# Kernel tuning notes

Hardware: AMD Instinct MI355X
Metric: run time of the kernel (lower is better)

The kernel has to match this reference:

```python
import jax, jax.numpy as jnp
import numpy as np

B, T, C = 2, 2048, 2048
H, HKV = 32, 8
D = C // H            # head_dim = 64
G = H // HKV          # groups = 4
ROPE_BASE = 10000.0


def _rotate_half(x):
    x1, x2 = jnp.split(x, 2, axis=-1)
    return jnp.concatenate((-x2, x1), axis=-1)


def _rope_tables(seq_len, dim):
    inv_freq = 1.0 / (ROPE_BASE ** (jnp.arange(0, dim, 2, dtype=jnp.float32) / dim))
    t = jnp.arange(seq_len, dtype=jnp.float32)
    freqs = jnp.outer(t, inv_freq)          # [T, D/2]
    emb = jnp.concatenate((freqs, freqs), axis=-1)  # [T, D]
    return jnp.cos(emb), jnp.sin(emb)


def setup_inputs() -> dict:
    key = jax.random.key(0)
    ks = jax.random.split(key, 5)
    s = 0.02
    return {
        "x": jax.random.normal(ks[0], (B, T, C), jnp.float32),
        "Wq": jax.random.normal(ks[1], (C, C), jnp.float32) * s,
        "Wk": jax.random.normal(ks[2], (HKV * D, C), jnp.float32) * s,
        "Wv": jax.random.normal(ks[3], (HKV * D, C), jnp.float32) * s,
        "Wo": jax.random.normal(ks[4], (C, C), jnp.float32) * s,
    }


def reference(x, Wq, Wk, Wv, Wo):
    b, t, c = x.shape
    # fused QKV projections (nn.Linear: y = x @ W.T)
    q = (x @ Wq.T).reshape(b, t, H, D).transpose(0, 2, 1, 3)      # [B,H,T,D]
    k = (x @ Wk.T).reshape(b, t, HKV, D).transpose(0, 2, 1, 3)    # [B,HKV,T,D]
    v = (x @ Wv.T).reshape(b, t, HKV, D).transpose(0, 2, 1, 3)

    # RoPE (start_pos = 0)
    cos, sin = _rope_tables(t, D)           # [T, D] each
    cos = cos[None, None]                   # [1,1,T,D]
    sin = sin[None, None]
    q = q * cos + _rotate_half(q) * sin
    k = k * cos + _rotate_half(k) * sin

    # GQA head expansion (repeat_interleave on head dim)
    k = jnp.repeat(k, G, axis=1)            # [B,H,T,D]
    v = jnp.repeat(v, G, axis=1)

    # causal attention
    scale = 1.0 / jnp.sqrt(jnp.asarray(D, jnp.float32))
    scores = jnp.einsum('bhqd,bhkd->bhqk', q, k) * scale          # [B,H,T,T]
    causal = jnp.tril(jnp.ones((t, t), dtype=bool))
    scores = jnp.where(causal[None, None], scores, -jnp.inf)
    attn = jax.nn.softmax(scores.astype(jnp.float32), axis=-1).astype(q.dtype)
    out = jnp.einsum('bhqk,bhkd->bhqd', attn, v)                  # [B,H,T,D]
    out = out.transpose(0, 2, 1, 3).reshape(b, t, c)
    return out @ Wo.T
```

## Files before the change

### kernel.cpp

```cpp
#include <hip/hip_runtime.h>
#include <hip/hip_bf16.h>
#include <math.h>

typedef short short8 __attribute__((ext_vector_type(8)));
typedef float floatx4 __attribute__((ext_vector_type(4)));
typedef unsigned int uintx4 __attribute__((ext_vector_type(4)));
typedef int intx2 __attribute__((ext_vector_type(2)));

typedef __attribute__((address_space(1))) unsigned int as1_u32;
typedef __attribute__((address_space(3))) unsigned int as3_u32;

__device__ __forceinline__ void load_lds16(const void* g, void* l) {
  __builtin_amdgcn_global_load_lds((const as1_u32*)g, (as3_u32*)l, 16, 0, 0);
}

__device__ __forceinline__ unsigned short f2bf(float f) {
  __bf16 h = (__bf16)f;
  return __builtin_bit_cast(unsigned short, h);
}

__device__ __forceinline__ unsigned int pack_bf16(float a, float b) {
  return (unsigned int)f2bf(a) | ((unsigned int)f2bf(b) << 16);
}

#define MFMA16(a, b, c) __builtin_amdgcn_mfma_f32_16x16x32_bf16(a, b, c, 0, 0, 0)

#define TB 2
#define TT 2048
#define TC 2048
#define QKN 2560
#define KOFF 2048
#define SCALE_Q 0.18033688f

__global__ __launch_bounds__(256) void cast_all(
    const float* __restrict__ x, const float* __restrict__ wq,
    const float* __restrict__ wk, const float* __restrict__ wv,
    const float* __restrict__ wo,
    unsigned short* __restrict__ xb, unsigned short* __restrict__ wqkv,
    unsigned short* __restrict__ wob, float2* __restrict__ ropeTab) {
  if (blockIdx.x < 256) {
    const int idx = blockIdx.x * 256 + threadIdx.x;
    const int t = idx >> 5, d = idx & 31;
    const float inv = exp2f((float)d * -0.4152410119f);
    float sn, cs;
    sincosf((float)t * inv, &sn, &cs);
    ropeTab[idx] = make_float2(cs, sn);
  }
  long i4 = (long)blockIdx.x * 256 + threadIdx.x;
  const float* src;
  unsigned short* dst;
  if (i4 < 2097152)      { src = x;  dst = xb; }
  else if (i4 < 3145728) { src = wq; dst = wqkv;           i4 -= 2097152; }
  else if (i4 < 3407872) { src = wk; dst = wqkv + 4194304; i4 -= 3145728; }
  else if (i4 < 3670016) { src = wv; dst = wqkv + 5242880; i4 -= 3407872; }
  else                   { src = wo; dst = wob;            i4 -= 3670016; }
  float4 v = ((const float4*)src)[i4];
  ushort4 o;
  o.x = f2bf(v.x); o.y = f2bf(v.y); o.z = f2bf(v.z); o.w = f2bf(v.w);
  ((ushort4*)dst)[i4] = o;
}

#define MFMA_QUAD(I0, J0, BF)                                                  \
  __builtin_amdgcn_s_setprio(1);                                               \
  _Pragma("unroll") for (int i_ = 0; i_ < 4; ++i_) {                           \
    _Pragma("unroll") for (int j_ = 0; j_ < 2; ++j_) {                         \
      acc[(I0) + i_][(J0) + j_] =                                              \
          MFMA16(af[i_][0], BF[j_][0], acc[(I0) + i_][(J0) + j_]);             \
      acc[(I0) + i_][(J0) + j_] =                                              \
          MFMA16(af[i_][1], BF[j_][1], acc[(I0) + i_][(J0) + j_]);             \
    }                                                                          \
  }                                                                            \
  __builtin_amdgcn_s_setprio(0);

__device__ __forceinline__ void gemm256_8ph(
    const unsigned short* __restrict__ A, const unsigned short* __restrict__ Bw,
    char* dynlds, int m0, int n0, int K, floatx4 (&acc)[8][4]) {
  const int tid = threadIdx.x;
  const int lane = tid & 63;
  const int w = tid >> 6;
  const int quad = lane >> 4, l15 = lane & 15;
  const int wm = w >> 2, wn = w & 3;

  const int srow8 = tid >> 3;
  const int schk = (tid & 7) ^ (srow8 & 7);
  const unsigned short* aS = A + (size_t)(m0 + srow8) * K + schk * 8;
  const unsigned short* bS = Bw + (size_t)(n0 + srow8) * K + schk * 8;

  const int key0 = (quad ^ (l15 & 7)) << 4;
  const int key1 = ((4 + quad) ^ (l15 & 7)) << 4;
  const int rdA = (wm * 16 + l15) * 128;
  const int rdB = 32768 + ((wn >> 1) * 64 + (wn & 1) * 16 + l15) * 128;

  const int NIT = K >> 7;

  auto stage = [&](int bb, int isB, int h, int tt) {
    char* d = dynlds + bb * 65536 + isB * 32768 + h * 16384;
    const unsigned short* s = (isB ? bS : aS) + (size_t)tt * 64 + (size_t)(h * 128) * K;
    load_lds16(s, d + tid * 16);
    load_lds16(s + (size_t)64 * K, d + 8192 + tid * 16);
  };

  stage(0, 0, 0, 0); stage(0, 1, 0, 0); stage(0, 1, 1, 0); stage(0, 0, 1, 0);
  stage(1, 0, 0, 1); stage(1, 1, 1, 1);
  asm volatile("s_waitcnt vmcnt(4)" ::: "memory");
  __builtin_amdgcn_s_barrier();

  short8 af[4][2], bfA[2][2], bfB[2][2];
  const char* cb0 = dynlds;
  const char* cb1 = dynlds + 65536;

  for (int it = 0; it < NIT; ++it) {
    const int tO = it * 2 + 1, tE2 = it * 2 + 2, tO2 = it * 2 + 3;
    const bool STG = (it < NIT - 1);

#pragma unroll
    for (int i = 0; i < 4; ++i) {
      af[i][0] = *(const short8*)(cb0 + rdA + i * 4096 + key0);
      af[i][1] = *(const short8*)(cb0 + rdA + i * 4096 + key1);
    }
#pragma unroll
    for (int j = 0; j < 2; ++j) {
      bfA[j][0] = *(const short8*)(cb0 + rdB + j * 4096 + key0);
      bfA[j][1] = *(const short8*)(cb0 + rdB + j * 4096 + key1);
    }
    stage(1, 1, 0, tO);
    __builtin_amdgcn_s_barrier();
    asm volatile("s_waitcnt lgkmcnt(0)" ::: "memory");
    MFMA_QUAD(0, 0, bfA)
    __builtin_amdgcn_s_barrier();

#pragma unroll
    for (int j = 0; j < 2; ++j) {
      bfB[j][0] = *(const short8*)(cb0 + rdB + 16384 + j * 4096 + key0);
      bfB[j][1] = *(const short8*)(cb0 + rdB + 16384 + j * 4096 + key1);
    }
    stage(1, 0, 1, tO);
    __builtin_amdgcn_s_barrier();
    asm volatile("s_waitcnt lgkmcnt(0)" ::: "memory");
    MFMA_QUAD(0, 2, bfB)
    __builtin_amdgcn_s_barrier();

#pragma unroll
    for (int i = 0; i < 4; ++i) {
      af[i][0] = *(const short8*)(cb0 + rdA + (i + 4) * 4096 + key0);
      af[i][1] = *(const short8*)(cb0 + rdA + (i + 4) * 4096 + key1);
    }
    if (STG) stage(0, 0, 0, tE2);
    __builtin_amdgcn_s_barrier();
    asm volatile("s_waitcnt lgkmcnt(0)" ::: "memory");
    MFMA_QUAD(4, 2, bfB)
    __builtin_amdgcn_s_barrier();

    if (STG) stage(0, 1, 1, tE2);
    MFMA_QUAD(4, 0, bfA)
    if (STG) asm volatile("s_waitcnt vmcnt(4)" ::: "memory");
    else     asm volatile("s_waitcnt vmcnt(0)" ::: "memory");
    __builtin_amdgcn_s_barrier();

#pragma unroll
    for (int i = 0; i < 4; ++i) {
      af[i][0] = *(const short8*)(cb1 + rdA + i * 4096 + key0);
      af[i][1] = *(const short8*)(cb1 + rdA + i * 4096 + key1);
    }
#pragma unroll
    for (int j = 0; j < 2; ++j) {
      bfA[j][0] = *(const short8*)(cb1 + rdB + j * 4096 + key0);
      bfA[j][1] = *(const short8*)(cb1 + rdB + j * 4096 + key1);
    }
    if (STG) stage(0, 1, 0, tE2);
    __builtin_amdgcn_s_barrier();
    asm volatile("s_waitcnt lgkmcnt(0)" ::: "memory");
    MFMA_QUAD(0, 0, bfA)
    __builtin_amdgcn_s_barrier();

#pragma unroll
    for (int j = 0; j < 2; ++j) {
      bfB[j][0] = *(const short8*)(cb1 + rdB + 16384 + j * 4096 + key0);
      bfB[j][1] = *(const short8*)(cb1 + rdB + 16384 + j * 4096 + key1);
    }
    if (STG) stage(0, 0, 1, tE2);
    __builtin_amdgcn_s_barrier();
    asm volatile("s_waitcnt lgkmcnt(0)" ::: "memory");
    MFMA_QUAD(0, 2, bfB)
    __builtin_amdgcn_s_barrier();

#pragma unroll
    for (int i = 0; i < 4; ++i) {
      af[i][0] = *(const short8*)(cb1 + rdA + (i + 4) * 4096 + key0);
      af[i][1] = *(const short8*)(cb1 + rdA + (i + 4) * 4096 + key1);
    }
    if (STG) stage(1, 0, 0, tO2);
    __builtin_amdgcn_s_barrier();
    asm volatile("s_waitcnt lgkmcnt(0)" ::: "memory");
    MFMA_QUAD(4, 2, bfB)
    __builtin_amdgcn_s_barrier();

    if (STG) stage(1, 1, 1, tO2);
    MFMA_QUAD(4, 0, bfA)
    if (STG) asm volatile("s_waitcnt vmcnt(4)" ::: "memory");
    else     asm volatile("s_waitcnt vmcnt(0)" ::: "memory");
    __builtin_amdgcn_s_barrier();
  }
}

#define OUTCOL(n0, wn, j, l15) \
  ((n0) + ((j) >> 1) * 128 + ((wn) >> 1) * 64 + ((wn) & 1) * 16 + ((j) & 1) * 32 + (l15))

__global__ __launch_bounds__(512, 2) void gemm_qkv(const unsigned short* __restrict__ A,
                                                   const unsigned short* __restrict__ Bw,
                                                   unsigned short* __restrict__ qk,
                                                   unsigned short* __restrict__ vT,
                                                   const float2* __restrict__ ropeTab) {
  extern __shared__ char dynlds[];
  const int K = 2048;
  const int tid = threadIdx.x;
  const int lane = tid & 63, w = tid >> 6;
  const int quad = lane >> 4, l15 = lane & 15;
  const int wm = w >> 2, wn = w & 3;

  const int lin = blockIdx.y * 12 + blockIdx.x;
  const int wg = (lin & 7) * 24 + (lin >> 3);
  const int m0 = (wg / 12) * 256;
  const int n0 = (wg % 12) * 256;

  floatx4 acc[8][4];
#pragma unroll
  for (int i = 0; i < 8; ++i)
#pragma unroll
    for (int j = 0; j < 4; ++j) acc[i][j] = (floatx4){0.f, 0.f, 0.f, 0.f};

  gemm256_8ph(A, Bw, dynlds, m0, n0, K, acc);

  if (n0 < QKN) {
    const float qscale = (n0 < KOFF) ? SCALE_Q : 1.0f;
    const int d = (wn & 1) * 16 + l15;
#pragma unroll
    for (int i = 0; i < 8; ++i) {
      const int rowb = m0 + i * 32 + wm * 16 + quad * 4;
      const int tb = rowb & (TT - 1);
#pragma unroll
      for (int jp = 0; jp < 4; jp += 2) {
        const int col = OUTCOL(n0, wn, jp, l15);
#pragma unroll
        for (int r = 0; r < 4; ++r) {
          const float2 cssn = ropeTab[(tb + r) * 32 + d];
          const float a = acc[i][jp][r], b2 = acc[i][jp + 1][r];
          const float qa = (a * cssn.x - b2 * cssn.y) * qscale;
          const float qb = (b2 * cssn.x + a * cssn.y) * qscale;
          unsigned short* p = qk + (size_t)(rowb + r) * QKN + col;
          p[0] = f2bf(qa);
          p[32] = f2bf(qb);
        }
      }
    }
  } else {
#pragma unroll
    for (int i = 0; i < 8; ++i) {
      const int rowb = m0 + i * 32 + wm * 16 + quad * 4;
#pragma unroll
      for (int j = 0; j < 4; ++j) {
        const int col = OUTCOL(n0, wn, j, l15);
        ushort4 pk;
        pk.x = f2bf(acc[i][j][0]); pk.y = f2bf(acc[i][j][1]);
        pk.z = f2bf(acc[i][j][2]); pk.w = f2bf(acc[i][j][3]);
        *(ushort4*)(vT + (size_t)(col - 2560) * 4096 + rowb) = pk;
      }
    }
  }
}

__global__ __launch_bounds__(512, 2) void gemm_nt_f32(const unsigned short* __restrict__ A,
                                                      const unsigned short* __restrict__ Bw,
                                                      float* __restrict__ C,
                                                      int M, int N, int Kdim) {
  extern __shared__ char dynlds[];
  const int K = 2048;
  const int tid = threadIdx.x;
  const int lane = tid & 63, w = tid >> 6;
  const int quad = lane >> 4, l15 = lane & 15;
  const int wm = w >> 2, wn = w & 3;

  const int lin = blockIdx.y * 8 + blockIdx.x;
  const int wg = (lin & 7) * 16 + (lin >> 3);
  const int m0 = (wg >> 3) * 256;
  const int n0 = (wg & 7) * 256;

  floatx4 acc[8][4];
#pragma unroll
  for (int i = 0; i < 8; ++i)
#pragma unroll
    for (int j = 0; j < 4; ++j) acc[i][j] = (floatx4){0.f, 0.f, 0.f, 0.f};

  gemm256_8ph(A, Bw, dynlds, m0, n0, K, acc);

#pragma unroll
  for (int i = 0; i < 8; ++i) {
    const int row = m0 + i * 32 + wm * 16 + quad * 4;
#pragma unroll
    for (int j = 0; j < 4; ++j) {
      const int col = OUTCOL(n0, wn, j, l15);
#pragma unroll
      for (int r = 0; r < 4; ++r)
        C[(size_t)(row + r) * N + col] = acc[i][j][r];
    }
  }
}

__global__ __launch_bounds__(256, 3) void attn_kernel(const unsigned short* __restrict__ qk,
                                                      const unsigned short* __restrict__ vT,
                                                      unsigned short* __restrict__ attn) {
  const int h = blockIdx.x, b = blockIdx.y;
  const int qt = 15 - (int)blockIdx.z;
  const int hk = h >> 2;
  const int tid = threadIdx.x;
  const int w = tid >> 6, lane = tid & 63, quad = lane >> 4, l15 = lane & 15;

  __shared__ char lds[32768];

  const int srow = tid >> 3;
  const int sgrp = ((tid & 7) ^ (srow & 7));
  const int relbase = w * 32 + l15;

  const short8 ones = {16256, 16256, 16256, 16256, 16256, 16256, 16256, 16256};

  const size_t rowQ = (size_t)(b * TT + qt * 128);

  {
    const unsigned short* qsrc = qk + (rowQ + srow) * QKN + h * 64 + sgrp * 8;
#pragma unroll
    for (int p = 0; p < 4; ++p)
      load_lds16(qsrc + (size_t)p * 32 * QKN, lds + p * 4096 + tid * 16);
  }
  __syncthreads();
  short8 qf[2][2];
#pragma unroll
  for (int i = 0; i < 2; ++i)
#pragma unroll
    for (int ks = 0; ks < 2; ++ks)
      qf[i][ks] = *(const short8*)(lds + (w * 32 + i * 16 + l15) * 128 +
                                   ((((ks << 2) + quad) ^ (l15 & 7)) << 4));
  __syncthreads();

  floatx4 accO[2][4], accL[2];
#pragma unroll
  for (int i = 0; i < 2; ++i) {
    accL[i] = (floatx4){0.f, 0.f, 0.f, 0.f};
#pragma unroll
    for (int j = 0; j < 4; ++j) accO[i][j] = (floatx4){0.f, 0.f, 0.f, 0.f};
  }

  const unsigned short* kptr =
      qk + (size_t)(b * TT + srow) * QKN + KOFF + hk * 64 + sgrp * 8;
  const unsigned short* vptr =
      vT + (size_t)(hk * 64 + srow) * 4096 + b * TT + sgrp * 8;

  load_lds16(kptr, lds + tid * 16);
  load_lds16(kptr + (size_t)32 * QKN, lds + 4096 + tid * 16);
  load_lds16(vptr, lds + 16384 + tid * 16);
  load_lds16(vptr + (size_t)32 * 4096, lds + 16384 + 4096 + tid * 16);
  kptr += (size_t)64 * QKN;
  vptr += 64;
  __syncthreads();

  auto step = [&](const int BUF, const bool PREF, const int MREL) {
    if (PREF) {
      char* kd = lds + ((BUF ^ 1) * 8192);
      char* vd = lds + 16384 + ((BUF ^ 1) * 8192);
      load_lds16(kptr, kd + tid * 16);
      load_lds16(kptr + (size_t)32 * QKN, kd + 4096 + tid * 16);
      load_lds16(vptr, vd + tid * 16);
      load_lds16(vptr + (size_t)32 * 4096, vd + 4096 + tid * 16);
      kptr += (size_t)64 * QKN;
      vptr += 64;
    }

    const char* Ks = lds + BUF * 8192;
    floatx4 st[2][4];
    __builtin_amdgcn_s_setprio(1);
#pragma unroll
    for (int jm = 0; jm < 4; ++jm) {
      const int krow = jm * 16 + l15;
      const short8 kf0 = *(const short8*)(Ks + krow * 128 + ((quad ^ (l15 & 7)) << 4));
      const short8 kf1 = *(const short8*)(Ks + krow * 128 + (((4 + quad) ^ (l15 & 7)) << 4));
#pragma unroll
      for (int i = 0; i < 2; ++i) {
        floatx4 z = (floatx4){0.f, 0.f, 0.f, 0.f};
        z = __builtin_amdgcn_mfma_f32_16x16x32_bf16(kf0, qf[i][0], z, 0, 0, 0);
        st[i][jm] = __builtin_amdgcn_mfma_f32_16x16x32_bf16(kf1, qf[i][1], z, 0, 0, 0);
      }
    }
    __builtin_amdgcn_s_setprio(0);

    const char* Vt = lds + 16384 + BUF * 8192;
    short8 vf[2][4];
#pragma unroll
    for (int ks = 0; ks < 2; ++ks)
#pragma unroll
      for (int jd = 0; jd < 4; ++jd) {
        const int d = jd * 16 + l15;
        vf[ks][jd] = *(const short8*)(Vt + d * 128 +
                                      ((((ks << 2) + quad) ^ (l15 & 7)) << 4));
      }

    short8 pT[2][2];
#pragma unroll
    for (int i = 0; i < 2; ++i) {
      unsigned int U[4][2];
#pragma unroll
      for (int jm = 0; jm < 4; ++jm) {
        float e0 = __builtin_amdgcn_exp2f(st[i][jm][0]);
        float e1 = __builtin_amdgcn_exp2f(st[i][jm][1]);
        float e2 = __builtin_amdgcn_exp2f(st[i][jm][2]);
        float e3 = __builtin_amdgcn_exp2f(st[i][jm][3]);
        if (MREL >= 0) {
          const int rel = relbase + i * 16 - MREL;
          const int kg = jm * 16 + quad * 4;
          if (kg > rel) e0 = 0.f;
          if (kg + 1 > rel) e1 = 0.f;
          if (kg + 2 > rel) e2 = 0.f;
          if (kg + 3 > rel) e3 = 0.f;
        }
        U[jm][0] = pack_bf16(e0, e1);
        U[jm][1] = pack_bf16(e2, e3);
      }
#pragma unroll
      for (int ks = 0; ks < 2; ++ks) {
        uintx4 t;
#pragma unroll
        for (int hh = 0; hh < 2; ++hh) {
          intx2 r32 = __builtin_amdgcn_permlane32_swap(
              (int)U[2 * ks][hh], (int)U[2 * ks + 1][hh], false, false);
          intx2 r16 = __builtin_amdgcn_permlane16_swap(r32[0], r32[1], false, false);
          t[hh] = (unsigned int)r16[0];
          t[2 + hh] = (unsigned int)r16[1];
        }
        pT[i][ks] = __builtin_bit_cast(short8, t);
      }
    }

    __builtin_amdgcn_s_setprio(1);
#pragma unroll
    for (int ks = 0; ks < 2; ++ks) {
      accL[0] = __builtin_amdgcn_mfma_f32_16x16x32_bf16(pT[0][ks], ones, accL[0], 0, 0, 0);
      accL[1] = __builtin_amdgcn_mfma_f32_16x16x32_bf16(pT[1][ks], ones, accL[1], 0, 0, 0);
#pragma unroll
      for (int jd = 0; jd < 4; ++jd) {
        accO[0][jd] = __builtin_amdgcn_mfma_f32_16x16x32_bf16(pT[0][ks], vf[ks][jd], accO[0][jd], 0, 0, 0);
        accO[1][jd] = __builtin_amdgcn_mfma_f32_16x16x32_bf16(pT[1][ks], vf[ks][jd], accO[1][jd], 0, 0, 0);
      }
    }
    __builtin_amdgcn_s_setprio(0);
    __syncthreads();
  };

  for (int t2 = 0; t2 < qt; ++t2) {
    step(0, true, -1);
    step(1, true, -1);
  }
  step(0, true, 0);
  step(1, false, 64);

#pragma unroll
  for (int i2 = 0; i2 < 2; ++i2) {
    floatx4 rl;
#pragma unroll
    for (int r = 0; r < 4; ++r) rl[r] = __builtin_amdgcn_rcpf(accL[i2][r]);
#pragma unroll
    for (int jd = 0; jd < 4; ++jd) {
      const int col = h * 64 + jd * 16 + l15;
#pragma unroll
      for (int r = 0; r < 4; ++r) {
        const size_t row = rowQ + w * 32 + i2 * 16 + quad * 4 + r;
        attn[row * TC + col] = f2bf(accO[i2][jd][r] * rl[r]);
      }
    }
  }
}

extern "C" void kernel_launch(void* const* d_in, const int* in_sizes, int n_in,
                              void* d_out, int out_size, void* d_ws, size_t ws_size,
                              hipStream_t stream) {
  const float* x = (const float*)d_in[0];
  const float* Wq = (const float*)d_in[1];
  const float* Wk = (const float*)d_in[2];
  const float* Wv = (const float*)d_in[3];
  const float* Wo = (const float*)d_in[4];
  float* out = (float*)d_out;

  char* ws = (char*)d_ws;
  unsigned short* xb   = (unsigned short*)(ws);
  unsigned short* wqkv = (unsigned short*)(ws + 16777216);
  unsigned short* wob  = (unsigned short*)(ws + 29360128);
  unsigned short* qk   = (unsigned short*)(ws + 37748736);
  unsigned short* vT   = (unsigned short*)(ws + 58720256);
  unsigned short* attn = (unsigned short*)(ws + 62914560);
  float2* ropeTab = (float2*)(ws + 62914560);

  cast_all<<<18432, 256, 0, stream>>>(x, Wq, Wk, Wv, Wo, xb, wqkv, wob, ropeTab);
  gemm_qkv<<<dim3(12, 16), 512, 131072, stream>>>(xb, wqkv, qk, vT, ropeTab);
  attn_kernel<<<dim3(32, 2, 16), 256, 0, stream>>>(qk, vT, attn);
  gemm_nt_f32<<<dim3(8, 16), 512, 131072, stream>>>(attn, wob, out, 4096, TC, 2048);
}
```

Measured before the change: 263.9 us.

## Software-pipeline LDS fragment reads ahead of MFMAs in GEMM mainloop

```diff
diff --git a/kernel.cpp b/kernel.cpp
--- a/kernel.cpp
+++ b/kernel.cpp
@@ -60,17 +60,29 @@
   ((ushort4*)dst)[i4] = o;
 }
 
-#define MFMA_QUAD(I0, J0, BF)                                                  \
+#define MFMA_Q(AF, I0, J0, BF)                                                 \
   __builtin_amdgcn_s_setprio(1);                                               \
   _Pragma("unroll") for (int i_ = 0; i_ < 4; ++i_) {                           \
     _Pragma("unroll") for (int j_ = 0; j_ < 2; ++j_) {                         \
       acc[(I0) + i_][(J0) + j_] =                                              \
-          MFMA16(af[i_][0], BF[j_][0], acc[(I0) + i_][(J0) + j_]);             \
+          MFMA16(AF[i_][0], BF[j_][0], acc[(I0) + i_][(J0) + j_]);             \
       acc[(I0) + i_][(J0) + j_] =                                              \
-          MFMA16(af[i_][1], BF[j_][1], acc[(I0) + i_][(J0) + j_]);             \
+          MFMA16(AF[i_][1], BF[j_][1], acc[(I0) + i_][(J0) + j_]);             \
     }                                                                          \
   }                                                                            \
   __builtin_amdgcn_s_setprio(0);
+
+#define RD_A(DST, CB, OFS)                                                     \
+  _Pragma("unroll") for (int i_ = 0; i_ < 4; ++i_) {                           \
+    DST[i_][0] = *(const short8*)((CB) + rdA + ((OFS) + i_) * 4096 + key0);    \
+    DST[i_][1] = *(const short8*)((CB) + rdA + ((OFS) + i_) * 4096 + key1);    \
+  }
+
+#define RD_B(DST, CB, OFS)                                                     \
+  _Pragma("unroll") for (int j_ = 0; j_ < 2; ++j_) {                           \
+    DST[j_][0] = *(const short8*)((CB) + rdB + (OFS) + j_ * 4096 + key0);      \
+    DST[j_][1] = *(const short8*)((CB) + rdB + (OFS) + j_ * 4096 + key1);      \
+  }
 
 __device__ __forceinline__ void gemm256_8ph(
     const unsigned short* __restrict__ A, const unsigned short* __restrict__ Bw,
@@ -104,101 +116,81 @@
   stage(1, 0, 0, 1); stage(1, 1, 1, 1);
   asm volatile("s_waitcnt vmcnt(4)" ::: "memory");
   __builtin_amdgcn_s_barrier();
-
-  short8 af[4][2], bfA[2][2], bfB[2][2];
+  asm volatile("" ::: "memory");
+
+  short8 afLo[4][2], afHi[4][2], bfAe[2][2], bfAo[2][2], bfB[2][2];
   const char* cb0 = dynlds;
   const char* cb1 = dynlds + 65536;
+
+  RD_A(afLo, cb0, 0)
+  RD_B(bfAe, cb0, 0)
 
   for (int it = 0; it < NIT; ++it) {
     const int tO = it * 2 + 1, tE2 = it * 2 + 2, tO2 = it * 2 + 3;
     const bool STG = (it < NIT - 1);
 
-#pragma unroll
-    for (int i = 0; i < 4; ++i) {
-      af[i][0] = *(const short8*)(cb0 + rdA + i * 4096 + key0);
-      af[i][1] = *(const short8*)(cb0 + rdA + i * 4096 + key1);
-    }
-#pragma unroll
-    for (int j = 0; j < 2; ++j) {
-      bfA[j][0] = *(const short8*)(cb0 + rdB + j * 4096 + key0);
-      bfA[j][1] = *(const short8*)(cb0 + rdB + j * 4096 + key1);
-    }
     stage(1, 1, 0, tO);
-    __builtin_amdgcn_s_barrier();
+    RD_B(bfB, cb0, 16384)
+    asm volatile("s_waitcnt lgkmcnt(4)" ::: "memory");
+    MFMA_Q(afLo, 0, 0, bfAe)
+    __builtin_amdgcn_s_barrier();
+
+    stage(1, 0, 1, tO);
+    RD_A(afHi, cb0, 4)
+    asm volatile("s_waitcnt lgkmcnt(8)" ::: "memory");
+    MFMA_Q(afLo, 0, 2, bfB)
+    __builtin_amdgcn_s_barrier();
+
+    if (STG) stage(0, 0, 0, tE2);
     asm volatile("s_waitcnt lgkmcnt(0)" ::: "memory");
-    MFMA_QUAD(0, 0, bfA)
-    __builtin_amdgcn_s_barrier();
-
-#pragma unroll
-    for (int j = 0; j < 2; ++j) {
-      bfB[j][0] = *(const short8*)(cb0 + rdB + 16384 + j * 4096 + key0);
-      bfB[j][1] = *(const short8*)(cb0 + rdB + 16384 + j * 4096 + key1);
-    }
-    stage(1, 0, 1, tO);
-    __builtin_amdgcn_s_barrier();
+    MFMA_Q(afHi, 4, 2, bfB)
+    __builtin_amdgcn_s_barrier();
+
+    if (STG) {
+      stage(0, 1, 1, tE2);
+      asm volatile("s_waitcnt vmcnt(4)" ::: "memory");
+    } else {
+      asm volatile("s_waitcnt vmcnt(0)" ::: "memory");
+    }
+    __builtin_amdgcn_s_barrier();
+    asm volatile("" ::: "memory");
+    RD_A(afLo, cb1, 0)
+    RD_B(bfAo, cb1, 0)
+    __builtin_amdgcn_sched_barrier(0);
+    MFMA_Q(afHi, 4, 0, bfAe)
+    __builtin_amdgcn_s_barrier();
+
+    if (STG) stage(0, 1, 0, tE2);
+    RD_B(bfB, cb1, 16384)
+    asm volatile("s_waitcnt lgkmcnt(4)" ::: "memory");
+    MFMA_Q(afLo, 0, 0, bfAo)
+    __builtin_amdgcn_s_barrier();
+
+    if (STG) stage(0, 0, 1, tE2);
+    RD_A(afHi, cb1, 4)
+    asm volatile("s_waitcnt lgkmcnt(8)" ::: "memory");
+    MFMA_Q(afLo, 0, 2, bfB)
+    __builtin_amdgcn_s_barrier();
+
+    if (STG) stage(1, 0, 0, tO2);
     asm volatile("s_waitcnt lgkmcnt(0)" ::: "memory");
-    MFMA_QUAD(0, 2, bfB)
-    __builtin_amdgcn_s_barrier();
-
-#pragma unroll
-    for (int i = 0; i < 4; ++i) {
-      af[i][0] = *(const short8*)(cb0 + rdA + (i + 4) * 4096 + key0);
-      af[i][1] = *(const short8*)(cb0 + rdA + (i + 4) * 4096 + key1);
-    }
-    if (STG) stage(0, 0, 0, tE2);
-    __builtin_amdgcn_s_barrier();
-    asm volatile("s_waitcnt lgkmcnt(0)" ::: "memory");
-    MFMA_QUAD(4, 2, bfB)
-    __builtin_amdgcn_s_barrier();
-
-    if (STG) stage(0, 1, 1, tE2);
-    MFMA_QUAD(4, 0, bfA)
-    if (STG) asm volatile("s_waitcnt vmcnt(4)" ::: "memory");
-    else     asm volatile("s_waitcnt vmcnt(0)" ::: "memory");
-    __builtin_amdgcn_s_barrier();
-
-#pragma unroll
-    for (int i = 0; i < 4; ++i) {
-      af[i][0] = *(const short8*)(cb1 + rdA + i * 4096 + key0);
-      af[i][1] = *(const short8*)(cb1 + rdA + i * 4096 + key1);
-    }
-#pragma unroll
-    for (int j = 0; j < 2; ++j) {
-      bfA[j][0] = *(const short8*)(cb1 + rdB + j * 4096 + key0);
-      bfA[j][1] = *(const short8*)(cb1 + rdB + j * 4096 + key1);
-    }
-    if (STG) stage(0, 1, 0, tE2);
-    __builtin_amdgcn_s_barrier();
-    asm volatile("s_waitcnt lgkmcnt(0)" ::: "memory");
-    MFMA_QUAD(0, 0, bfA)
-    __builtin_amdgcn_s_barrier();
-
-#pragma unroll
-    for (int j = 0; j < 2; ++j) {
-      bfB[j][0] = *(const short8*)(cb1 + rdB + 16384 + j * 4096 + key0);
-      bfB[j][1] = *(const short8*)(cb1 + rdB + 16384 + j * 4096 + key1);
-    }
-    if (STG) stage(0, 0, 1, tE2);
-    __builtin_amdgcn_s_barrier();
-    asm volatile("s_waitcnt lgkmcnt(0)" ::: "memory");
-    MFMA_QUAD(0, 2, bfB)
-    __builtin_amdgcn_s_barrier();
-
-#pragma unroll
-    for (int i = 0; i < 4; ++i) {
-      af[i][0] = *(const short8*)(cb1 + rdA + (i + 4) * 4096 + key0);
-      af[i][1] = *(const short8*)(cb1 + rdA + (i + 4) * 4096 + key1);
-    }
-    if (STG) stage(1, 0, 0, tO2);
-    __builtin_amdgcn_s_barrier();
-    asm volatile("s_waitcnt lgkmcnt(0)" ::: "memory");
-    MFMA_QUAD(4, 2, bfB)
-    __builtin_amdgcn_s_barrier();
-
-    if (STG) stage(1, 1, 1, tO2);
-    MFMA_QUAD(4, 0, bfA)
-    if (STG) asm volatile("s_waitcnt vmcnt(4)" ::: "memory");
-    else     asm volatile("s_waitcnt vmcnt(0)" ::: "memory");
+    MFMA_Q(afHi, 4, 2, bfB)
+    __builtin_amdgcn_s_barrier();
+
+    if (STG) {
+      stage(1, 1, 1, tO2);
+      asm volatile("s_waitcnt vmcnt(4)" ::: "memory");
+    } else {
+      asm volatile("s_waitcnt vmcnt(0)" ::: "memory");
+    }
+    __builtin_amdgcn_s_barrier();
+    asm volatile("" ::: "memory");
+    if (STG) {
+      RD_A(afLo, cb0, 0)
+      RD_B(bfAe, cb0, 0)
+      __builtin_amdgcn_sched_barrier(0);
+    }
+    MFMA_Q(afHi, 4, 0, bfAo)
     __builtin_amdgcn_s_barrier();
   }
 }
@@ -206,7 +198,7 @@
 #define OUTCOL(n0, wn, j, l15) \
   ((n0) + ((j) >> 1) * 128 + ((wn) >> 1) * 64 + ((wn) & 1) * 16 + ((j) & 1) * 32 + (l15))
 
-__global__ __launch_bounds__(512, 2) void gemm_qkv(const unsigned short* __restrict__ A,
+__global__ __launch_bounds__(512, 1) void gemm_qkv(const unsigned short* __restrict__ A,
                                                    const unsigned short* __restrict__ Bw,
                                                    unsigned short* __restrict__ qk,
                                                    unsigned short* __restrict__ vT,
@@ -269,7 +261,7 @@
   }
 }
 
-__global__ __launch_bounds__(512, 2) void gemm_nt_f32(const unsigned short* __restrict__ A,
+__global__ __launch_bounds__(512, 1) void gemm_nt_f32(const unsigned short* __restrict__ A,
                                                       const unsigned short* __restrict__ Bw,
                                                       float* __restrict__ C,
                                                       int M, int N, int Kdim) {
```

Result: slower. 289.4 us (+9.6%).

## Retile output projection GEMM to 256x128 tiles with custom double-buffered pipeline

Applied to the files above, without the earlier changes.

```diff
diff --git a/kernel.cpp b/kernel.cpp
--- a/kernel.cpp
+++ b/kernel.cpp
@@ -269,6 +269,16 @@
   }
 }
 
+#define NT_MFMA(J0, BF)                                                        \
+  __builtin_amdgcn_s_setprio(1);                                               \
+  _Pragma("unroll") for (int i_ = 0; i_ < 4; ++i_) {                           \
+    _Pragma("unroll") for (int j_ = 0; j_ < 2; ++j_) {                         \
+      acc[i_][(J0) + j_] = MFMA16(af[i_][0], BF[j_][0], acc[i_][(J0) + j_]);   \
+      acc[i_][(J0) + j_] = MFMA16(af[i_][1], BF[j_][1], acc[i_][(J0) + j_]);   \
+    }                                                                          \
+  }                                                                            \
+  __builtin_amdgcn_s_setprio(0);
+
 __global__ __launch_bounds__(512, 2) void gemm_nt_f32(const unsigned short* __restrict__ A,
                                                       const unsigned short* __restrict__ Bw,
                                                       float* __restrict__ C,
@@ -278,27 +288,122 @@
   const int tid = threadIdx.x;
   const int lane = tid & 63, w = tid >> 6;
   const int quad = lane >> 4, l15 = lane & 15;
-  const int wm = w >> 2, wn = w & 3;
-
-  const int lin = blockIdx.y * 8 + blockIdx.x;
-  const int wg = (lin & 7) * 16 + (lin >> 3);
-  const int m0 = (wg >> 3) * 256;
-  const int n0 = (wg & 7) * 256;
-
-  floatx4 acc[8][4];
-#pragma unroll
-  for (int i = 0; i < 8; ++i)
+  const int wm = w >> 1, wn = w & 1;
+
+  const int lin = blockIdx.y * 16 + blockIdx.x;
+  const int wg = (lin & 7) * 32 + (lin >> 3);
+  const int m0 = (wg >> 4) * 256;
+  const int n0 = (wg & 15) * 128;
+
+  floatx4 acc[4][4];
+#pragma unroll
+  for (int i = 0; i < 4; ++i)
 #pragma unroll
     for (int j = 0; j < 4; ++j) acc[i][j] = (floatx4){0.f, 0.f, 0.f, 0.f};
 
-  gemm256_8ph(A, Bw, dynlds, m0, n0, K, acc);
-
-#pragma unroll
-  for (int i = 0; i < 8; ++i) {
-    const int row = m0 + i * 32 + wm * 16 + quad * 4;
+  const int srow8 = tid >> 3;
+  const int schk = (tid & 7) ^ (srow8 & 7);
+  const unsigned short* aS = A + (size_t)(m0 + srow8) * K + schk * 8;
+  const unsigned short* bS = Bw + (size_t)(n0 + srow8) * K + schk * 8;
+
+  const int key0 = (quad ^ (l15 & 7)) << 4;
+  const int key1 = ((4 + quad) ^ (l15 & 7)) << 4;
+  const int rdA = (wm * 64 + l15) * 128;
+  const int rdB = 32768 + (wn * 64 + l15) * 128;
+
+  auto stage = [&](int bb, int slot, int tt) {
+    char* d = dynlds + bb * 49152 + slot * 16384;
+    const unsigned short* s =
+        (slot == 2 ? bS : aS + (size_t)(slot * 128) * K) + (size_t)tt * 64;
+    load_lds16(s, d + tid * 16);
+    load_lds16(s + (size_t)64 * K, d + 8192 + tid * 16);
+  };
+
+  stage(0, 0, 0); stage(0, 1, 0); stage(0, 2, 0);
+  stage(1, 0, 1); stage(1, 1, 1);
+  asm volatile("s_waitcnt vmcnt(4)" ::: "memory");
+  __builtin_amdgcn_s_barrier();
+
+  short8 af[4][2], bfL[2][2], bfR[2][2];
+  const char* cb0 = dynlds;
+  const char* cb1 = dynlds + 49152;
+  const int NIT = K >> 7;
+
+  for (int it = 0; it < NIT; ++it) {
+    const int tO = it * 2 + 1, tE2 = it * 2 + 2, tO2 = it * 2 + 3;
+    const bool STG = (it < NIT - 1);
+
+#pragma unroll
+    for (int i = 0; i < 4; ++i) {
+      af[i][0] = *(const short8*)(cb0 + rdA + i * 2048 + key0);
+      af[i][1] = *(const short8*)(cb0 + rdA + i * 2048 + key1);
+    }
+#pragma unroll
+    for (int j = 0; j < 2; ++j) {
+      bfL[j][0] = *(const short8*)(cb0 + rdB + j * 2048 + key0);
+      bfL[j][1] = *(const short8*)(cb0 + rdB + j * 2048 + key1);
+    }
+    stage(1, 2, tO);
+    __builtin_amdgcn_s_barrier();
+    asm volatile("s_waitcnt lgkmcnt(0)" ::: "memory");
+    NT_MFMA(0, bfL)
+    __builtin_amdgcn_s_barrier();
+
+#pragma unroll
+    for (int j = 0; j < 2; ++j) {
+      bfR[j][0] = *(const short8*)(cb0 + rdB + (2 + j) * 2048 + key0);
+      bfR[j][1] = *(const short8*)(cb0 + rdB + (2 + j) * 2048 + key1);
+    }
+    if (STG) {
+      stage(0, 0, tE2); stage(0, 1, tE2);
+      asm volatile("s_waitcnt vmcnt(4)" ::: "memory");
+    } else {
+      asm volatile("s_waitcnt vmcnt(0)" ::: "memory");
+    }
+    __builtin_amdgcn_s_barrier();
+    asm volatile("s_waitcnt lgkmcnt(0)" ::: "memory");
+    NT_MFMA(2, bfR)
+    __builtin_amdgcn_s_barrier();
+
+#pragma unroll
+    for (int i = 0; i < 4; ++i) {
+      af[i][0] = *(const short8*)(cb1 + rdA + i * 2048 + key0);
+      af[i][1] = *(const short8*)(cb1 + rdA + i * 2048 + key1);
+    }
+#pragma unroll
+    for (int j = 0; j < 2; ++j) {
+      bfL[j][0] = *(const short8*)(cb1 + rdB + j * 2048 + key0);
+      bfL[j][1] = *(const short8*)(cb1 + rdB + j * 2048 + key1);
+    }
+    if (STG) stage(0, 2, tE2);
+    __builtin_amdgcn_s_barrier();
+    asm volatile("s_waitcnt lgkmcnt(0)" ::: "memory");
+    NT_MFMA(0, bfL)
+    __builtin_amdgcn_s_barrier();
+
+#pragma unroll
+    for (int j = 0; j < 2; ++j) {
+      bfR[j][0] = *(const short8*)(cb1 + rdB + (2 + j) * 2048 + key0);
+      bfR[j][1] = *(const short8*)(cb1 + rdB + (2 + j) * 2048 + key1);
+    }
+    if (STG) {
+      stage(1, 0, tO2); stage(1, 1, tO2);
+      asm volatile("s_waitcnt vmcnt(4)" ::: "memory");
+    } else {
+      asm volatile("s_waitcnt vmcnt(0)" ::: "memory");
+    }
+    __builtin_amdgcn_s_barrier();
+    asm volatile("s_waitcnt lgkmcnt(0)" ::: "memory");
+    NT_MFMA(2, bfR)
+    __builtin_amdgcn_s_barrier();
+  }
+
+#pragma unroll
+  for (int i = 0; i < 4; ++i) {
+    const int row = m0 + wm * 64 + i * 16 + quad * 4;
 #pragma unroll
     for (int j = 0; j < 4; ++j) {
-      const int col = OUTCOL(n0, wn, j, l15);
+      const int col = n0 + wn * 64 + j * 16 + l15;
 #pragma unroll
       for (int r = 0; r < 4; ++r)
         C[(size_t)(row + r) * N + col] = acc[i][j][r];
@@ -499,5 +604,5 @@
   cast_all<<<18432, 256, 0, stream>>>(x, Wq, Wk, Wv, Wo, xb, wqkv, wob, ropeTab);
   gemm_qkv<<<dim3(12, 16), 512, 131072, stream>>>(xb, wqkv, qk, vT, ropeTab);
   attn_kernel<<<dim3(32, 2, 16), 256, 0, stream>>>(qk, vT, attn);
-  gemm_nt_f32<<<dim3(8, 16), 512, 131072, stream>>>(attn, wob, out, 4096, TC, 2048);
-}
+  gemm_nt_f32<<<dim3(16, 16), 512, 98304, stream>>>(attn, wob, out, 4096, TC, 2048);
+}
```

Result: faster. 249.3 us (-5.6%).
